# Kernel optimization log

Measured on AMD Instinct MI355X. Metric: run time of the kernel, lower is better.

## Reference

```python
import jax, jax.numpy as jnp
import numpy as np

N = 20000          # num_nodes
R = 48             # num_relations
NB = 12            # num_bases
E = 640000         # num_edges (avg degree 32)
INIT, M1, M2 = 128, 128, 128
OUT3 = 512 - M2 - M1 - INIT  # = 128, per output_size arithmetic in __init__


def setup_inputs() -> dict:
    key = jax.random.key(0)
    ks = jax.random.split(key, 20)
    p = lambda k, shape, s=0.05: jax.random.normal(k, shape, jnp.float32) * s
    return {
        "emb": p(ks[0], (N, INIT)),
        "edge_src": jax.random.randint(ks[1], (E,), 0, N),
        "edge_dst": jax.random.randint(ks[2], (E,), 0, N),
        "edge_types": jax.random.randint(ks[3], (E,), 0, R),
        "comp1": p(ks[4], (R, NB), 0.3), "basis1": p(ks[5], (NB, INIT, M1)),
        "root1": p(ks[6], (INIT, M1)), "bias1": jnp.zeros((M1,), jnp.float32),
        "comp2": p(ks[7], (R, NB), 0.3), "basis2": p(ks[8], (NB, M1, M2)),
        "root2": p(ks[9], (M1, M2)), "bias2": jnp.zeros((M2,), jnp.float32),
        "comp3": p(ks[10], (R, NB), 0.3), "basis3": p(ks[11], (NB, M2, OUT3)),
        "root3": p(ks[12], (M2, OUT3)), "bias3": jnp.zeros((OUT3,), jnp.float32),
    }


def rgcn_conv(x, src, dst, etype, comp, basis, root, bias):
    """PyG RGCNConv with basis decomposition and per-relation mean aggregation.
    out_i = bias + x_i @ root + sum_r W_r^T . mean_{j in N_r(i)} x_j
    Mean aggregation commutes with the linear map, so aggregate raw features per
    (relation, target) first, then apply the relation weights as one batched GEMM.
    """
    Fin = x.shape[1]
    W = jnp.einsum('rb,bio->rio', comp, basis)                 # [R, Fin, Fout]
    seg = etype * N + dst                                      # fused (rel, dst) id
    msg = jax.ops.segment_sum(x[src], seg, num_segments=R * N) # [R*N, Fin]
    cnt = jax.ops.segment_sum(jnp.ones((src.shape[0], 1), x.dtype), seg,
                              num_segments=R * N)
    agg = (msg / jnp.maximum(cnt, 1.0)).reshape(R, N, Fin)     # mean, 0 if no edges
    return jnp.einsum('rni,rio->no', agg, W) + x @ root + bias


def reference(emb, edge_src, edge_dst, edge_types,
              comp1, basis1, root1, bias1,
              comp2, basis2, root2, bias2,
              comp3, basis3, root3, bias3):
    x1 = jax.nn.relu(rgcn_conv(emb, edge_src, edge_dst, edge_types,
                               comp1, basis1, root1, bias1))
    x2 = jax.nn.relu(rgcn_conv(x1, edge_src, edge_dst, edge_types,
                               comp2, basis2, root2, bias2))
    x3 = jax.nn.relu(rgcn_conv(x2, edge_src, edge_dst, edge_types,
                               comp3, basis3, root3, bias3))
    # dropout(0.2) is identity in eval mode
    return jnp.concatenate((x3, x2, x1, emb), axis=1)          # [N, 512]
```

## Files before the change

kernel.cpp:

```cpp
#include <hip/hip_runtime.h>
#include <hip/hip_bf16.h>

#define N_NODES 20000
#define R_REL   48
#define NBASES  12
#define E_EDGES 640000
#define KDIM    1664
#define KSTEPS  52
#define SLOTS   96
#define PF      8

typedef __attribute__((ext_vector_type(8))) short bf16x8;
typedef __attribute__((ext_vector_type(4))) float f32x4;

__device__ inline float loadF(const void* p, long long idx, int isf32) {
    if (isf32 != 0) return ((const float*)p)[idx];
    return __bfloat162float(((const __hip_bfloat16*)p)[idx]);
}

__device__ inline void storeF(void* p, long long idx, int isf32, float v) {
    if (isf32 != 0) ((float*)p)[idx] = v;
    else ((__hip_bfloat16*)p)[idx] = __float2bfloat16(v);
}

__global__ void detect_dtype(const void* emb, int* flag) {
    if (threadIdx.x == 0 && blockIdx.x == 0) {
        const unsigned short* h = (const unsigned short*)emb;
        int f32 = 0;
        for (int k = 0; k < 256; k++) {
            unsigned int bits = ((unsigned int)h[k]) << 16;
            float v = __uint_as_float(bits);
            if (!(fabsf(v) < 1000.0f)) f32 = 1;
        }
        *flag = f32;
    }
}

__global__ void zero_i32(int* p, int n) {
    int i = blockIdx.x * 256 + threadIdx.x;
    if (i < n) p[i] = 0;
}

__global__ void scatter_d96(const int* src, const int* dst, const int* typ,
                            int* cursordP, int* s_pack) {
    int e = blockIdx.x * 256 + threadIdx.x;
    if (e < E_EDGES) {
        int d = dst[e];
        int pos = atomicAdd(&cursordP[d * 32], 1);
        if (pos < SLOTS)
            s_pack[d * SLOTS + pos] = src[e] | (typ[e] << 20);
    }
}

__global__ void build_wcat3(const void* b0, const void* r0,
                            const void* b1, const void* r1,
                            const void* b2, const void* r2,
                            __hip_bfloat16* Wt, const int* flagp) {
    int l = blockIdx.z;
    const void* basis = (l == 0) ? b0 : (l == 1) ? b1 : b2;
    const void* root  = (l == 0) ? r0 : (l == 1) ? r1 : r2;
    int o = blockIdx.x;
    int k = blockIdx.y * 256 + threadIdx.x;
    if (k >= KDIM) return;
    int isf32 = *flagp;
    float v;
    if (k < NBASES * 128) {
        int b = k >> 7, i = k & 127;
        v = loadF(basis, b * 16384 + i * 128 + o, isf32);
    } else {
        v = loadF(root, (k - NBASES * 128) * 128 + o, isf32);
    }
    Wt[(long long)l * (128 * KDIM) + (long long)o * KDIM + k] =
        __float2bfloat16(v);
}

#define FB(j, idx) do {                                                       \
    int p_ = spkw[idx];                                                       \
    pp[j] = p_;                                                               \
    sxp[j] = *(const unsigned int*)                                           \
             (xp + (long long)(p_ & 0xFFFFF) * xld + col);                    \
} while (0)

#define CB(j) do {                                                            \
    int rel_ = pp[j] >> 20;                                                   \
    const float* cp_ = &scSw[rel_ * NBASES];                                  \
    float4 cA_ = *(const float4*)cp_;                                         \
    float4 cB_ = *(const float4*)(cp_ + 4);                                   \
    float4 cC_ = *(const float4*)(cp_ + 8);                                   \
    float x0_ = __uint_as_float(sxp[j] << 16);                                \
    float x1_ = __uint_as_float(sxp[j] & 0xFFFF0000u);                        \
    accA[0]  += cA_.x * x0_;  accB[0]  += cA_.x * x1_;                        \
    accA[1]  += cA_.y * x0_;  accB[1]  += cA_.y * x1_;                        \
    accA[2]  += cA_.z * x0_;  accB[2]  += cA_.z * x1_;                        \
    accA[3]  += cA_.w * x0_;  accB[3]  += cA_.w * x1_;                        \
    accA[4]  += cB_.x * x0_;  accB[4]  += cB_.x * x1_;                        \
    accA[5]  += cB_.y * x0_;  accB[5]  += cB_.y * x1_;                        \
    accA[6]  += cB_.z * x0_;  accB[6]  += cB_.z * x1_;                        \
    accA[7]  += cB_.w * x0_;  accB[7]  += cB_.w * x1_;                        \
    accA[8]  += cC_.x * x0_;  accB[8]  += cC_.x * x1_;                        \
    accA[9]  += cC_.y * x0_;  accB[9]  += cC_.y * x1_;                        \
    accA[10] += cC_.z * x0_;  accB[10] += cC_.z * x1_;                        \
    accA[11] += cC_.w * x0_;  accB[11] += cC_.w * x1_;                        \
} while (0)

__global__ __launch_bounds__(256, 6) void aggregate_bf16(
        const int* s_pack, const int* cntP, const void* comp,
        const void* x, int xbase, int xld,
        unsigned short* A, const int* flagp) {
    if (*flagp != 0) return;
    __shared__ float scomp[R_REL * NBASES];
    __shared__ float scS[4][R_REL * NBASES];
    __shared__ int   shcnt[4][R_REL];
    __shared__ int   spk[4][64];
    int tid = threadIdx.x;
    int lane = tid & 63;
    int w = tid >> 6;
    int dstn = blockIdx.x * 4 + w;

    for (int i = tid; i < R_REL * NBASES; i += 256)
        scomp[i] = __bfloat162float(((const __hip_bfloat16*)comp)[i]);
    __syncthreads();

    const unsigned short* xp = (const unsigned short*)x + xbase;
    int cnt = cntP[dstn * 32]; if (cnt > SLOTS) cnt = SLOTS;
    int e0 = dstn * SLOTS;
    int e1 = e0 + cnt;
    int col = lane * 2;
    int* spkw = spk[w];
    float* scSw = scS[w];

    if (lane < R_REL) shcnt[w][lane] = 0;
    asm volatile("s_waitcnt lgkmcnt(0)" ::: "memory");
    for (int c0 = e0; c0 < e1; c0 += 64) {
        int e = c0 + lane;
        int p = s_pack[(e < e1) ? e : (e1 - 1)];
        if (c0 == e0) spkw[lane] = p;
        if (e < e1) atomicAdd(&shcnt[w][p >> 20], 1);
    }
    asm volatile("s_waitcnt lgkmcnt(0) vmcnt(0)" ::: "memory");
    if (lane < R_REL) {
        int c = shcnt[w][lane];
        float iv = (c > 0) ? (1.0f / (float)c) : 0.0f;
#pragma unroll
        for (int b = 0; b < NBASES; b++)
            scSw[lane * NBASES + b] = scomp[lane * NBASES + b] * iv;
    }
    asm volatile("s_waitcnt lgkmcnt(0)" ::: "memory");

    float accA[NBASES], accB[NBASES];
#pragma unroll
    for (int b = 0; b < NBASES; b++) { accA[b] = 0.0f; accB[b] = 0.0f; }

    for (int c0 = e0; c0 < e1; c0 += 64) {
        if (c0 != e0) {
            int e = c0 + lane;
            spkw[lane] = s_pack[(e < e1) ? e : (e1 - 1)];
        }
        asm volatile("s_waitcnt lgkmcnt(0)" ::: "memory");
        int cn = e1 - c0; if (cn > 64) cn = 64;
        unsigned int sxp[PF]; int pp[PF];
#pragma unroll
        for (int j = 0; j < PF; j++)
            if (j < cn) FB(j, j);
        int i2 = 0;
        for (; i2 + PF <= cn; i2 += PF) {
#pragma unroll
            for (int j = 0; j < PF; j++) {
                CB(j);
                if (i2 + j + PF < cn) FB(j, i2 + j + PF);
            }
        }
#pragma unroll
        for (int j = 0; j < PF; j++)
            if (i2 + j < cn) CB(j);
    }

    unsigned short* Ar = A + (long long)dstn * KDIM;
#pragma unroll
    for (int b = 0; b < NBASES; b++) {
        __hip_bfloat16 h0 = __float2bfloat16(accA[b]);
        __hip_bfloat16 h1 = __float2bfloat16(accB[b]);
        unsigned int pk = ((unsigned int)*(unsigned short*)&h1 << 16) |
                          (unsigned int)*(unsigned short*)&h0;
        *(unsigned int*)(Ar + b * 128 + col) = pk;
    }
    *(unsigned int*)(Ar + NBASES * 128 + col) =
        *(const unsigned int*)(xp + (long long)dstn * xld + col);
}

#define FX(j, idx) do {                                                       \
    int p_ = spkw[idx];                                                       \
    pp[j] = p_;                                                               \
    sx[j] = *(const float2*)(xp + (long long)(p_ & 0xFFFFF) * xld + col);     \
} while (0)

#define CX(j) do {                                                            \
    int rel_ = pp[j] >> 20;                                                   \
    const float* cp_ = &scSw[rel_ * NBASES];                                  \
    float4 cA_ = *(const float4*)cp_;                                         \
    float4 cB_ = *(const float4*)(cp_ + 4);                                   \
    float4 cC_ = *(const float4*)(cp_ + 8);                                   \
    float x0_ = sx[j].x, x1_ = sx[j].y;                                       \
    accA[0]  += cA_.x * x0_;  accB[0]  += cA_.x * x1_;                        \
    accA[1]  += cA_.y * x0_;  accB[1]  += cA_.y * x1_;                        \
    accA[2]  += cA_.z * x0_;  accB[2]  += cA_.z * x1_;                        \
    accA[3]  += cA_.w * x0_;  accB[3]  += cA_.w * x1_;                        \
    accA[4]  += cB_.x * x0_;  accB[4]  += cB_.x * x1_;                        \
    accA[5]  += cB_.y * x0_;  accB[5]  += cB_.y * x1_;                        \
    accA[6]  += cB_.z * x0_;  accB[6]  += cB_.z * x1_;                        \
    accA[7]  += cB_.w * x0_;  accB[7]  += cB_.w * x1_;                        \
    accA[8]  += cC_.x * x0_;  accB[8]  += cC_.x * x1_;                        \
    accA[9]  += cC_.y * x0_;  accB[9]  += cC_.y * x1_;                        \
    accA[10] += cC_.z * x0_;  accB[10] += cC_.z * x1_;                        \
    accA[11] += cC_.w * x0_;  accB[11] += cC_.w * x1_;                        \
} while (0)

__global__ __launch_bounds__(256) void aggregate_f32(
        const int* s_pack, const int* cntP, const void* comp,
        const void* x, int xbase, int xld,
        unsigned short* A, const int* flagp) {
    if (*flagp == 0) return;
    __shared__ float scomp[R_REL * NBASES];
    __shared__ float scS[4][R_REL * NBASES];
    __shared__ int   shcnt[4][R_REL];
    __shared__ int   spk[4][64];
    int tid = threadIdx.x;
    int lane = tid & 63;
    int w = tid >> 6;
    int dstn = blockIdx.x * 4 + w;

    for (int i = tid; i < R_REL * NBASES; i += 256)
        scomp[i] = ((const float*)comp)[i];
    __syncthreads();

    const float* xp = (const float*)x + xbase;
    int cnt = cntP[dstn * 32]; if (cnt > SLOTS) cnt = SLOTS;
    int e0 = dstn * SLOTS;
    int e1 = e0 + cnt;
    int col = lane * 2;
    int* spkw = spk[w];
    float* scSw = scS[w];

    if (lane < R_REL) shcnt[w][lane] = 0;
    asm volatile("s_waitcnt lgkmcnt(0)" ::: "memory");
    for (int c0 = e0; c0 < e1; c0 += 64) {
        int e = c0 + lane;
        int p = s_pack[(e < e1) ? e : (e1 - 1)];
        if (c0 == e0) spkw[lane] = p;
        if (e < e1) atomicAdd(&shcnt[w][p >> 20], 1);
    }
    asm volatile("s_waitcnt lgkmcnt(0) vmcnt(0)" ::: "memory");
    if (lane < R_REL) {
        int c = shcnt[w][lane];
        float iv = (c > 0) ? (1.0f / (float)c) : 0.0f;
#pragma unroll
        for (int b = 0; b < NBASES; b++)
            scSw[lane * NBASES + b] = scomp[lane * NBASES + b] * iv;
    }
    asm volatile("s_waitcnt lgkmcnt(0)" ::: "memory");

    float accA[NBASES], accB[NBASES];
#pragma unroll
    for (int b = 0; b < NBASES; b++) { accA[b] = 0.0f; accB[b] = 0.0f; }

    for (int c0 = e0; c0 < e1; c0 += 64) {
        if (c0 != e0) {
            int e = c0 + lane;
            spkw[lane] = s_pack[(e < e1) ? e : (e1 - 1)];
        }
        asm volatile("s_waitcnt lgkmcnt(0)" ::: "memory");
        int cn = e1 - c0; if (cn > 64) cn = 64;
        float2 sx[PF]; int pp[PF];
#pragma unroll
        for (int j = 0; j < PF; j++)
            if (j < cn) FX(j, j);
        int i2 = 0;
        for (; i2 + PF <= cn; i2 += PF) {
#pragma unroll
            for (int j = 0; j < PF; j++) {
                CX(j);
                if (i2 + j + PF < cn) FX(j, i2 + j + PF);
            }
        }
#pragma unroll
        for (int j = 0; j < PF; j++)
            if (i2 + j < cn) CX(j);
    }

    unsigned short* Ar = A + (long long)dstn * KDIM;
#pragma unroll
    for (int b = 0; b < NBASES; b++) {
        __hip_bfloat16 h0 = __float2bfloat16(accA[b]);
        __hip_bfloat16 h1 = __float2bfloat16(accB[b]);
        unsigned int pk = ((unsigned int)*(unsigned short*)&h1 << 16) |
                          (unsigned int)*(unsigned short*)&h0;
        *(unsigned int*)(Ar + b * 128 + col) = pk;
    }
    {
        float2 f = *(const float2*)(xp + (long long)dstn * xld + col);
        __hip_bfloat16 h0 = __float2bfloat16(f.x);
        __hip_bfloat16 h1 = __float2bfloat16(f.y);
        unsigned int pk = ((unsigned int)*(unsigned short*)&h1 << 16) |
                          (unsigned int)*(unsigned short*)&h0;
        *(unsigned int*)(Ar + NBASES * 128 + col) = pk;
    }
}

__global__ __launch_bounds__(256) void gemm_out(
        const __hip_bfloat16* A, const __hip_bfloat16* Wt,
        const void* bias, void* out, int slot, const int* flagp) {
    int isf32 = *flagp;
    int tid = threadIdx.x;
    int lane = tid & 63;
    int w = tid >> 6;
    int lr = lane & 15;
    int lk = lane >> 4;
    int colBase = w * 32;
    int nb = blockIdx.x;
    const __hip_bfloat16* a0p = A + (long long)(nb * 32 + lr) * KDIM;
    const __hip_bfloat16* a1p = a0p + 16 * KDIM;
    const __hip_bfloat16* w0p = Wt + (long long)(colBase + lr) * KDIM;
    const __hip_bfloat16* w1p = w0p + 16 * KDIM;
    f32x4 acc00 = {0.f, 0.f, 0.f, 0.f};
    f32x4 acc01 = {0.f, 0.f, 0.f, 0.f};
    f32x4 acc10 = {0.f, 0.f, 0.f, 0.f};
    f32x4 acc11 = {0.f, 0.f, 0.f, 0.f};
#pragma unroll 4
    for (int ks = 0; ks < KSTEPS; ks++) {
        int ko = ks * 32 + lk * 8;
        bf16x8 a0 = *(const bf16x8*)(a0p + ko);
        bf16x8 a1 = *(const bf16x8*)(a1p + ko);
        bf16x8 b0 = *(const bf16x8*)(w0p + ko);
        bf16x8 b1 = *(const bf16x8*)(w1p + ko);
        acc00 = __builtin_amdgcn_mfma_f32_16x16x32_bf16(a0, b0, acc00, 0, 0, 0);
        acc01 = __builtin_amdgcn_mfma_f32_16x16x32_bf16(a0, b1, acc01, 0, 0, 0);
        acc10 = __builtin_amdgcn_mfma_f32_16x16x32_bf16(a1, b0, acc10, 0, 0, 0);
        acc11 = __builtin_amdgcn_mfma_f32_16x16x32_bf16(a1, b1, acc11, 0, 0, 0);
    }
    float bi0 = loadF(bias, colBase + lr, isf32);
    float bi1 = loadF(bias, colBase + 16 + lr, isf32);
#pragma unroll
    for (int q = 0; q < 4; q++) {
        int row = lk * 4 + q;
        long long n0 = (long long)(nb * 32 + row) * 512 + slot;
        long long n1 = n0 + 16 * 512;
        storeF(out, n0 + colBase + lr,      isf32, fmaxf(acc00[q] + bi0, 0.0f));
        storeF(out, n0 + colBase + 16 + lr, isf32, fmaxf(acc01[q] + bi1, 0.0f));
        storeF(out, n1 + colBase + lr,      isf32, fmaxf(acc10[q] + bi0, 0.0f));
        storeF(out, n1 + colBase + 16 + lr, isf32, fmaxf(acc11[q] + bi1, 0.0f));
    }
}

__global__ void copy_emb(const void* emb, void* out, const int* flagp) {
    int idx = blockIdx.x * 256 + threadIdx.x;
    int n = idx >> 4;
    int c8 = (idx & 15) * 8;
    if (*flagp) {
        const float4* s = (const float4*)((const float*)emb +
                                          (long long)n * 128 + c8);
        float4* d = (float4*)((float*)out + (long long)n * 512 + 384 + c8);
        d[0] = s[0];
        d[1] = s[1];
    } else {
        const uint4* s = (const uint4*)((const unsigned short*)emb +
                                        (long long)n * 128 + c8);
        uint4* d = (uint4*)((unsigned short*)out +
                            (long long)n * 512 + 384 + c8);
        *d = *s;
    }
}

extern "C" void kernel_launch(void* const* d_in, const int* in_sizes, int n_in,
                              void* d_out, int out_size, void* d_ws, size_t ws_size,
                              hipStream_t stream) {
    const void* emb  = d_in[0];
    const int* esrc = (const int*)d_in[1];
    const int* edst = (const int*)d_in[2];
    const int* etyp = (const int*)d_in[3];
    const void* comp[3];
    const void* basis[3];
    const void* root[3];
    const void* bias[3];
    for (int l = 0; l < 3; l++) {
        comp[l]  = d_in[4 + l * 4];
        basis[l] = d_in[5 + l * 4];
        root[l]  = d_in[6 + l * 4];
        bias[l]  = d_in[7 + l * 4];
    }

    char* ws = (char*)d_ws;
    int*   flag     = (int*)(ws + 0);
    int*   s_pack   = (int*)(ws + 256);
    int*   cursordP = (int*)(ws + 7680256);
    __hip_bfloat16* Wt = (__hip_bfloat16*)(ws + 10240256);
    __hip_bfloat16* A  = (__hip_bfloat16*)(ws + 11518208);

    detect_dtype<<<1, 64, 0, stream>>>(emb, flag);
    zero_i32<<<2500, 256, 0, stream>>>(cursordP, N_NODES * 32);
    scatter_d96<<<2500, 256, 0, stream>>>(esrc, edst, etyp, cursordP, s_pack);
    copy_emb<<<1250, 256, 0, stream>>>(emb, d_out, flag);
    build_wcat3<<<dim3(128, 7, 3), 256, 0, stream>>>(
        basis[0], root[0], basis[1], root[1], basis[2], root[2], Wt, flag);

    const void* xin = emb;
    int xbase = 0;
    int xld = 128;
    const int slots[3] = {256, 128, 0};
    for (int l = 0; l < 3; l++) {
        const __hip_bfloat16* Wtl = Wt + (long long)l * (128 * KDIM);
        aggregate_bf16<<<5000, 256, 0, stream>>>(s_pack, cursordP, comp[l],
                                                 xin, xbase, xld,
                                                 (unsigned short*)A, flag);
        aggregate_f32<<<5000, 256, 0, stream>>>(s_pack, cursordP, comp[l],
                                                xin, xbase, xld,
                                                (unsigned short*)A, flag);
        gemm_out<<<625, 256, 0, stream>>>(A, Wtl, bias[l], d_out,
                                          slots[l], flag);
        xin = d_out;
        xbase = slots[l];
        xld = 512;
    }
    (void)in_sizes; (void)n_in; (void)out_size; (void)ws_size;
}
```

Baseline: 596.1 us.

## Gather from compact bf16 feature copy and merge dtype-specific aggregate kernels

Adds a packed bf16 feature buffer, written by the embedding copy kernel and by the GEMM epilogue, so the neighbor aggregation always gathers dense bf16 rows instead of strided fp32 or bf16 rows from the output. The two dtype-specific aggregate kernels are merged into one, removing a launch per layer. It costs extra narrow scattered stores in the GEMM epilogue and more workspace, and drops the occupancy hint on the bf16 path.

```diff
diff --git a/kernel.cpp b/kernel.cpp
--- a/kernel.cpp
+++ b/kernel.cpp
@@ -21,6 +21,11 @@
 __device__ inline void storeF(void* p, long long idx, int isf32, float v) {
     if (isf32 != 0) ((float*)p)[idx] = v;
     else ((__hip_bfloat16*)p)[idx] = __float2bfloat16(v);
+}
+
+__device__ inline unsigned short toBf(float v) {
+    __hip_bfloat16 h = __float2bfloat16(v);
+    return *(unsigned short*)&h;
 }
 
 __global__ void detect_dtype(const void* emb, int* flag) {
@@ -74,11 +79,36 @@
         __float2bfloat16(v);
 }
 
+__global__ void copy_emb_xc(const void* emb, void* out, unsigned short* xc,
+                            const int* flagp) {
+    int idx = blockIdx.x * 256 + threadIdx.x;
+    int n = idx >> 4;
+    int c8 = (idx & 15) * 8;
+    if (*flagp) {
+        const float4* s = (const float4*)((const float*)emb +
+                                          (long long)n * 128 + c8);
+        float4 f0 = s[0], f1 = s[1];
+        float4* d = (float4*)((float*)out + (long long)n * 512 + 384 + c8);
+        d[0] = f0;
+        d[1] = f1;
+        ushort4 p0, p1;
+        p0.x = toBf(f0.x); p0.y = toBf(f0.y); p0.z = toBf(f0.z); p0.w = toBf(f0.w);
+        p1.x = toBf(f1.x); p1.y = toBf(f1.y); p1.z = toBf(f1.z); p1.w = toBf(f1.w);
+        *(ushort4*)(xc + (long long)n * 128 + c8) = p0;
+        *(ushort4*)(xc + (long long)n * 128 + c8 + 4) = p1;
+    } else {
+        uint4 v = *(const uint4*)((const unsigned short*)emb +
+                                  (long long)n * 128 + c8);
+        *(uint4*)((unsigned short*)out + (long long)n * 512 + 384 + c8) = v;
+        *(uint4*)(xc + (long long)n * 128 + c8) = v;
+    }
+}
+
 #define FB(j, idx) do {                                                       \
     int p_ = spkw[idx];                                                       \
     pp[j] = p_;                                                               \
     sxp[j] = *(const unsigned int*)                                           \
-             (xp + (long long)(p_ & 0xFFFFF) * xld + col);                    \
+             (xc + (long long)(p_ & 0xFFFFF) * 128 + col);                    \
 } while (0)
 
 #define CB(j) do {                                                            \
@@ -103,25 +133,23 @@
     accA[11] += cC_.w * x0_;  accB[11] += cC_.w * x1_;                        \
 } while (0)
 
-__global__ __launch_bounds__(256, 6) void aggregate_bf16(
+__global__ __launch_bounds__(256) void aggregate(
         const int* s_pack, const int* cntP, const void* comp,
-        const void* x, int xbase, int xld,
-        unsigned short* A, const int* flagp) {
-    if (*flagp != 0) return;
+        const unsigned short* xc, unsigned short* A, const int* flagp) {
     __shared__ float scomp[R_REL * NBASES];
     __shared__ float scS[4][R_REL * NBASES];
     __shared__ int   shcnt[4][R_REL];
     __shared__ int   spk[4][64];
+    int isf32 = *flagp;
     int tid = threadIdx.x;
     int lane = tid & 63;
     int w = tid >> 6;
     int dstn = blockIdx.x * 4 + w;
 
     for (int i = tid; i < R_REL * NBASES; i += 256)
-        scomp[i] = __bfloat162float(((const __hip_bfloat16*)comp)[i]);
+        scomp[i] = loadF(comp, i, isf32);
     __syncthreads();
 
-    const unsigned short* xp = (const unsigned short*)x + xbase;
     int cnt = cntP[dstn * 32]; if (cnt > SLOTS) cnt = SLOTS;
     int e0 = dstn * SLOTS;
     int e1 = e0 + cnt;
@@ -178,137 +206,18 @@
     unsigned short* Ar = A + (long long)dstn * KDIM;
 #pragma unroll
     for (int b = 0; b < NBASES; b++) {
-        __hip_bfloat16 h0 = __float2bfloat16(accA[b]);
-        __hip_bfloat16 h1 = __float2bfloat16(accB[b]);
-        unsigned int pk = ((unsigned int)*(unsigned short*)&h1 << 16) |
-                          (unsigned int)*(unsigned short*)&h0;
+        unsigned int pk = ((unsigned int)toBf(accB[b]) << 16) |
+                          (unsigned int)toBf(accA[b]);
         *(unsigned int*)(Ar + b * 128 + col) = pk;
     }
     *(unsigned int*)(Ar + NBASES * 128 + col) =
-        *(const unsigned int*)(xp + (long long)dstn * xld + col);
-}
-
-#define FX(j, idx) do {                                                       \
-    int p_ = spkw[idx];                                                       \
-    pp[j] = p_;                                                               \
-    sx[j] = *(const float2*)(xp + (long long)(p_ & 0xFFFFF) * xld + col);     \
-} while (0)
-
-#define CX(j) do {                                                            \
-    int rel_ = pp[j] >> 20;                                                   \
-    const float* cp_ = &scSw[rel_ * NBASES];                                  \
-    float4 cA_ = *(const float4*)cp_;                                         \
-    float4 cB_ = *(const float4*)(cp_ + 4);                                   \
-    float4 cC_ = *(const float4*)(cp_ + 8);                                   \
-    float x0_ = sx[j].x, x1_ = sx[j].y;                                       \
-    accA[0]  += cA_.x * x0_;  accB[0]  += cA_.x * x1_;                        \
-    accA[1]  += cA_.y * x0_;  accB[1]  += cA_.y * x1_;                        \
-    accA[2]  += cA_.z * x0_;  accB[2]  += cA_.z * x1_;                        \
-    accA[3]  += cA_.w * x0_;  accB[3]  += cA_.w * x1_;                        \
-    accA[4]  += cB_.x * x0_;  accB[4]  += cB_.x * x1_;                        \
-    accA[5]  += cB_.y * x0_;  accB[5]  += cB_.y * x1_;                        \
-    accA[6]  += cB_.z * x0_;  accB[6]  += cB_.z * x1_;                        \
-    accA[7]  += cB_.w * x0_;  accB[7]  += cB_.w * x1_;                        \
-    accA[8]  += cC_.x * x0_;  accB[8]  += cC_.x * x1_;                        \
-    accA[9]  += cC_.y * x0_;  accB[9]  += cC_.y * x1_;                        \
-    accA[10] += cC_.z * x0_;  accB[10] += cC_.z * x1_;                        \
-    accA[11] += cC_.w * x0_;  accB[11] += cC_.w * x1_;                        \
-} while (0)
-
-__global__ __launch_bounds__(256) void aggregate_f32(
-        const int* s_pack, const int* cntP, const void* comp,
-        const void* x, int xbase, int xld,
-        unsigned short* A, const int* flagp) {
-    if (*flagp == 0) return;
-    __shared__ float scomp[R_REL * NBASES];
-    __shared__ float scS[4][R_REL * NBASES];
-    __shared__ int   shcnt[4][R_REL];
-    __shared__ int   spk[4][64];
-    int tid = threadIdx.x;
-    int lane = tid & 63;
-    int w = tid >> 6;
-    int dstn = blockIdx.x * 4 + w;
-
-    for (int i = tid; i < R_REL * NBASES; i += 256)
-        scomp[i] = ((const float*)comp)[i];
-    __syncthreads();
-
-    const float* xp = (const float*)x + xbase;
-    int cnt = cntP[dstn * 32]; if (cnt > SLOTS) cnt = SLOTS;
-    int e0 = dstn * SLOTS;
-    int e1 = e0 + cnt;
-    int col = lane * 2;
-    int* spkw = spk[w];
-    float* scSw = scS[w];
-
-    if (lane < R_REL) shcnt[w][lane] = 0;
-    asm volatile("s_waitcnt lgkmcnt(0)" ::: "memory");
-    for (int c0 = e0; c0 < e1; c0 += 64) {
-        int e = c0 + lane;
-        int p = s_pack[(e < e1) ? e : (e1 - 1)];
-        if (c0 == e0) spkw[lane] = p;
-        if (e < e1) atomicAdd(&shcnt[w][p >> 20], 1);
-    }
-    asm volatile("s_waitcnt lgkmcnt(0) vmcnt(0)" ::: "memory");
-    if (lane < R_REL) {
-        int c = shcnt[w][lane];
-        float iv = (c > 0) ? (1.0f / (float)c) : 0.0f;
-#pragma unroll
-        for (int b = 0; b < NBASES; b++)
-            scSw[lane * NBASES + b] = scomp[lane * NBASES + b] * iv;
-    }
-    asm volatile("s_waitcnt lgkmcnt(0)" ::: "memory");
-
-    float accA[NBASES], accB[NBASES];
-#pragma unroll
-    for (int b = 0; b < NBASES; b++) { accA[b] = 0.0f; accB[b] = 0.0f; }
-
-    for (int c0 = e0; c0 < e1; c0 += 64) {
-        if (c0 != e0) {
-            int e = c0 + lane;
-            spkw[lane] = s_pack[(e < e1) ? e : (e1 - 1)];
-        }
-        asm volatile("s_waitcnt lgkmcnt(0)" ::: "memory");
-        int cn = e1 - c0; if (cn > 64) cn = 64;
-        float2 sx[PF]; int pp[PF];
-#pragma unroll
-        for (int j = 0; j < PF; j++)
-            if (j < cn) FX(j, j);
-        int i2 = 0;
-        for (; i2 + PF <= cn; i2 += PF) {
-#pragma unroll
-            for (int j = 0; j < PF; j++) {
-                CX(j);
-                if (i2 + j + PF < cn) FX(j, i2 + j + PF);
-            }
-        }
-#pragma unroll
-        for (int j = 0; j < PF; j++)
-            if (i2 + j < cn) CX(j);
-    }
-
-    unsigned short* Ar = A + (long long)dstn * KDIM;
-#pragma unroll
-    for (int b = 0; b < NBASES; b++) {
-        __hip_bfloat16 h0 = __float2bfloat16(accA[b]);
-        __hip_bfloat16 h1 = __float2bfloat16(accB[b]);
-        unsigned int pk = ((unsigned int)*(unsigned short*)&h1 << 16) |
-                          (unsigned int)*(unsigned short*)&h0;
-        *(unsigned int*)(Ar + b * 128 + col) = pk;
-    }
-    {
-        float2 f = *(const float2*)(xp + (long long)dstn * xld + col);
-        __hip_bfloat16 h0 = __float2bfloat16(f.x);
-        __hip_bfloat16 h1 = __float2bfloat16(f.y);
-        unsigned int pk = ((unsigned int)*(unsigned short*)&h1 << 16) |
-                          (unsigned int)*(unsigned short*)&h0;
-        *(unsigned int*)(Ar + NBASES * 128 + col) = pk;
-    }
+        *(const unsigned int*)(xc + (long long)dstn * 128 + col);
 }
 
 __global__ __launch_bounds__(256) void gemm_out(
         const __hip_bfloat16* A, const __hip_bfloat16* Wt,
-        const void* bias, void* out, int slot, const int* flagp) {
+        const void* bias, void* out, int slot,
+        unsigned short* xc, int writeXc, const int* flagp) {
     int isf32 = *flagp;
     int tid = threadIdx.x;
     int lane = tid & 63;
@@ -342,31 +251,24 @@
 #pragma unroll
     for (int q = 0; q < 4; q++) {
         int row = lk * 4 + q;
-        long long n0 = (long long)(nb * 32 + row) * 512 + slot;
-        long long n1 = n0 + 16 * 512;
-        storeF(out, n0 + colBase + lr,      isf32, fmaxf(acc00[q] + bi0, 0.0f));
-        storeF(out, n0 + colBase + 16 + lr, isf32, fmaxf(acc01[q] + bi1, 0.0f));
-        storeF(out, n1 + colBase + lr,      isf32, fmaxf(acc10[q] + bi0, 0.0f));
-        storeF(out, n1 + colBase + 16 + lr, isf32, fmaxf(acc11[q] + bi1, 0.0f));
-    }
-}
-
-__global__ void copy_emb(const void* emb, void* out, const int* flagp) {
-    int idx = blockIdx.x * 256 + threadIdx.x;
-    int n = idx >> 4;
-    int c8 = (idx & 15) * 8;
-    if (*flagp) {
-        const float4* s = (const float4*)((const float*)emb +
-                                          (long long)n * 128 + c8);
-        float4* d = (float4*)((float*)out + (long long)n * 512 + 384 + c8);
-        d[0] = s[0];
-        d[1] = s[1];
-    } else {
-        const uint4* s = (const uint4*)((const unsigned short*)emb +
-                                        (long long)n * 128 + c8);
-        uint4* d = (uint4*)((unsigned short*)out +
-                            (long long)n * 512 + 384 + c8);
-        *d = *s;
+        int r0 = nb * 32 + row;
+        int r1 = r0 + 16;
+        float v00 = fmaxf(acc00[q] + bi0, 0.0f);
+        float v01 = fmaxf(acc01[q] + bi1, 0.0f);
+        float v10 = fmaxf(acc10[q] + bi0, 0.0f);
+        float v11 = fmaxf(acc11[q] + bi1, 0.0f);
+        long long n0 = (long long)r0 * 512 + slot;
+        long long n1 = (long long)r1 * 512 + slot;
+        storeF(out, n0 + colBase + lr,      isf32, v00);
+        storeF(out, n0 + colBase + 16 + lr, isf32, v01);
+        storeF(out, n1 + colBase + lr,      isf32, v10);
+        storeF(out, n1 + colBase + 16 + lr, isf32, v11);
+        if (writeXc) {
+            xc[(long long)r0 * 128 + colBase + lr]      = toBf(v00);
+            xc[(long long)r0 * 128 + colBase + 16 + lr] = toBf(v01);
+            xc[(long long)r1 * 128 + colBase + lr]      = toBf(v10);
+            xc[(long long)r1 * 128 + colBase + 16 + lr] = toBf(v11);
+        }
     }
 }
 
@@ -393,32 +295,24 @@
     int*   s_pack   = (int*)(ws + 256);
     int*   cursordP = (int*)(ws + 7680256);
     __hip_bfloat16* Wt = (__hip_bfloat16*)(ws + 10240256);
-    __hip_bfloat16* A  = (__hip_bfloat16*)(ws + 11518208);
+    unsigned short* xc = (unsigned short*)(ws + 11518208);
+    unsigned short* A  = (unsigned short*)(ws + 16638208);
 
     detect_dtype<<<1, 64, 0, stream>>>(emb, flag);
     zero_i32<<<2500, 256, 0, stream>>>(cursordP, N_NODES * 32);
     scatter_d96<<<2500, 256, 0, stream>>>(esrc, edst, etyp, cursordP, s_pack);
-    copy_emb<<<1250, 256, 0, stream>>>(emb, d_out, flag);
+    copy_emb_xc<<<1250, 256, 0, stream>>>(emb, d_out, xc, flag);
     build_wcat3<<<dim3(128, 7, 3), 256, 0, stream>>>(
         basis[0], root[0], basis[1], root[1], basis[2], root[2], Wt, flag);
 
-    const void* xin = emb;
-    int xbase = 0;
-    int xld = 128;
     const int slots[3] = {256, 128, 0};
     for (int l = 0; l < 3; l++) {
         const __hip_bfloat16* Wtl = Wt + (long long)l * (128 * KDIM);
-        aggregate_bf16<<<5000, 256, 0, stream>>>(s_pack, cursordP, comp[l],
-                                                 xin, xbase, xld,
-                                                 (unsigned short*)A, flag);
-        aggregate_f32<<<5000, 256, 0, stream>>>(s_pack, cursordP, comp[l],
-                                                xin, xbase, xld,
-                                                (unsigned short*)A, flag);
-        gemm_out<<<625, 256, 0, stream>>>(A, Wtl, bias[l], d_out,
-                                          slots[l], flag);
-        xin = d_out;
-        xbase = slots[l];
-        xld = 512;
+        aggregate<<<5000, 256, 0, stream>>>(s_pack, cursordP, comp[l],
+                                            xc, A, flag);
+        gemm_out<<<625, 256, 0, stream>>>((const __hip_bfloat16*)A, Wtl,
+                                          bias[l], d_out, slots[l],
+                                          xc, (l < 2) ? 1 : 0, flag);
     }
     (void)in_sizes; (void)n_in; (void)out_size; (void)ws_size;
 }
```

Result: slower. 773.9 us (+29.8%).
